# Kernel tuning notes

Hardware: AMD Instinct MI355X
Metric: run time of the kernel (lower is better)

Reference implementation:

```python
import jax, jax.numpy as jnp
import numpy as np

MAX_DUR = 8  # exclusive upper bound used when sampling durations


def setup_inputs() -> dict:
    key = jax.random.key(0)
    k1, k2 = jax.random.split(key)
    B, S, D = 16, 512, 384
    text_emb = jax.random.normal(k1, (B, S, D), dtype=jnp.float32)
    durations = jax.random.randint(k2, (B, S), 0, MAX_DUR, dtype=jnp.int32)
    return {"text_emb": text_emb, "durations": durations}


def reference(text_emb, durations):
    # text_emb: [B, S, D] float32; durations: [B, S] int32
    B, S, D = text_emb.shape
    max_len = S * MAX_DUR  # static padded length (jit-compatible stand-in for pad_sequence)
    # cumulative end offset of each token's expanded span: [B, S]
    cs = jnp.cumsum(durations, axis=1)
    t = jnp.arange(max_len, dtype=cs.dtype)  # output frame positions
    # for each output frame t, source token idx = first j with cs[j] > t
    idx = jax.vmap(lambda c: jnp.searchsorted(c, t, side="right"))(cs)  # [B, max_len]
    total = cs[:, -1:]                      # [B, 1] total expanded length per batch
    valid = t[None, :] < total              # [B, max_len] padding mask
    idx = jnp.clip(idx, 0, S - 1)
    # gather embeddings: [B, max_len, D]
    out = jnp.take_along_axis(text_emb, idx[:, :, None], axis=1)
    return jnp.where(valid[:, :, None], out, jnp.zeros((), dtype=text_emb.dtype))
```

## Files before the change

### kernel.cpp

```cpp
#include <hip/hip_runtime.h>


#define BB 16
#define SS 512
#define DD 384
#define D4 (DD / 4)
#define MAXLEN 4096
#define BATCH_F4 (MAXLEN * D4)
#define K2_ITERS 8
#define K2_CHUNK (256 * K2_ITERS)
#define CHUNKS_PER_B (BATCH_F4 / K2_CHUNK)

typedef float f32x4 __attribute__((ext_vector_type(4)));

__global__ __launch_bounds__(256)
void lr_prologue_kernel(const int* __restrict__ dur, short* __restrict__ idxmap) {
    __shared__ int cs[SS];
    const int b       = blockIdx.x >> 2;
    const int quarter = blockIdx.x & 3;
    const int tid     = threadIdx.x;

    if (tid < 64) {
        const int* drow = dur + b * SS + tid * 8;
        int loc[8];
        int run = 0;
        #pragma unroll
        for (int j = 0; j < 8; ++j) { run += drow[j]; loc[j] = run; }
        int sc = run;
        #pragma unroll
        for (int off = 1; off < 64; off <<= 1) {
            int n = __shfl_up(sc, off, 64);
            if (tid >= off) sc += n;
        }
        const int base = sc - run;
        #pragma unroll
        for (int j = 0; j < 8; ++j) cs[tid * 8 + j] = base + loc[j];
    }
    __syncthreads();

    const int total = cs[SS - 1];
    short* omap = idxmap + b * MAXLEN + quarter * 1024;
    for (int k = 0; k < 4; ++k) {
        const int t = quarter * 1024 + k * 256 + tid;
        int lo = 0, hi = SS;
        while (lo < hi) {
            int mid = (lo + hi) >> 1;
            if (cs[mid] <= t) lo = mid + 1; else hi = mid;
        }
        if (lo > SS - 1) lo = SS - 1;
        omap[k * 256 + tid] = (short)((t < total) ? lo : -1);
    }
}

__global__ __launch_bounds__(256)
void lr_gather_kernel(const f32x4* __restrict__ emb,
                      const short* __restrict__ idxmap,
                      f32x4* __restrict__ out) {
    const unsigned x   = blockIdx.x;
    const unsigned xcd = x & 7;
    const unsigned w   = x >> 3;
    const unsigned b   = xcd + 8u * (w & 1);
    const unsigned c   = w >> 1;

    const unsigned local0 = c * K2_CHUNK + threadIdx.x;
    const f32x4* embb = emb + b * (SS * D4);
    const short* imap = idxmap + b * MAXLEN;
    f32x4* outb       = out + (size_t)b * BATCH_F4;

    #pragma unroll
    for (int k = 0; k < K2_ITERS; ++k) {
        const unsigned local = local0 + k * 256;
        const unsigned bt = local / D4;
        const unsigned d4 = local - bt * D4;
        const int idx = (int)imap[bt];
        f32x4 v = {0.f, 0.f, 0.f, 0.f};
        if (idx >= 0) v = embb[(unsigned)idx * D4 + d4];
        outb[local] = v;
    }
}

extern "C" void kernel_launch(void* const* d_in, const int* in_sizes, int n_in,
                              void* d_out, int out_size, void* d_ws, size_t ws_size,
                              hipStream_t stream) {
    const float* text_emb  = (const float*)d_in[0];
    const int*   durations = (const int*)d_in[1];
    float* out = (float*)d_out;

    short* idxmap = (short*)d_ws;

    lr_prologue_kernel<<<BB * 4, 256, 0, stream>>>(durations, idxmap);

    lr_gather_kernel<<<BB * CHUNKS_PER_B, 256, 0, stream>>>(
        (const f32x4*)text_emb, idxmap, (f32x4*)out);
}
```

Before: 119.1 us.

## Fuse duration prefix-sum and index search into the gather kernel

Merges the prologue and gather kernels into a single launch. Each gather block now recomputes the prefix sum of its batch row in shared memory and binary-searches only the handful of frame indices its chunk covers. This removes a kernel launch, the inter-kernel dependency and the global index-map round trip. In exchange, every block redundantly scans 512 durations, which adds per-block latency before any stores begin.

```diff
diff --git a/kernel.cpp b/kernel.cpp
--- a/kernel.cpp
+++ b/kernel.cpp
@@ -10,15 +10,23 @@
 #define K2_ITERS 8
 #define K2_CHUNK (256 * K2_ITERS)
 #define CHUNKS_PER_B (BATCH_F4 / K2_CHUNK)
+#define MAP_ENTRIES 24
 
 typedef float f32x4 __attribute__((ext_vector_type(4)));
 
 __global__ __launch_bounds__(256)
-void lr_prologue_kernel(const int* __restrict__ dur, short* __restrict__ idxmap) {
-    __shared__ int cs[SS];
-    const int b       = blockIdx.x >> 2;
-    const int quarter = blockIdx.x & 3;
-    const int tid     = threadIdx.x;
+void lr_fused_kernel(const int* __restrict__ dur,
+                     const f32x4* __restrict__ emb,
+                     f32x4* __restrict__ out) {
+    __shared__ int   cs[SS];
+    __shared__ short smap[MAP_ENTRIES];
+
+    const unsigned x   = blockIdx.x;
+    const unsigned xcd = x & 7;
+    const unsigned w   = x >> 3;
+    const unsigned b   = xcd + 8u * (w & 1);
+    const unsigned c   = w >> 1;
+    const int tid      = threadIdx.x;
 
     if (tid < 64) {
         const int* drow = dur + b * SS + tid * 8;
@@ -38,33 +46,25 @@
     }
     __syncthreads();
 
-    const int total = cs[SS - 1];
-    short* omap = idxmap + b * MAXLEN + quarter * 1024;
-    for (int k = 0; k < 4; ++k) {
-        const int t = quarter * 1024 + k * 256 + tid;
+    const unsigned base_f4 = c * K2_CHUNK;
+    const unsigned bt0     = base_f4 / D4;
+    const unsigned lastbt  = (base_f4 + K2_CHUNK - 1) / D4;
+    const unsigned nent    = lastbt - bt0 + 1;
+    const int total        = cs[SS - 1];
+    if (tid < (int)nent) {
+        const int t = (int)bt0 + tid;
         int lo = 0, hi = SS;
         while (lo < hi) {
             int mid = (lo + hi) >> 1;
             if (cs[mid] <= t) lo = mid + 1; else hi = mid;
         }
         if (lo > SS - 1) lo = SS - 1;
-        omap[k * 256 + tid] = (short)((t < total) ? lo : -1);
+        smap[tid] = (short)((t < total) ? lo : -1);
     }
-}
+    __syncthreads();
 
-__global__ __launch_bounds__(256)
-void lr_gather_kernel(const f32x4* __restrict__ emb,
-                      const short* __restrict__ idxmap,
-                      f32x4* __restrict__ out) {
-    const unsigned x   = blockIdx.x;
-    const unsigned xcd = x & 7;
-    const unsigned w   = x >> 3;
-    const unsigned b   = xcd + 8u * (w & 1);
-    const unsigned c   = w >> 1;
-
-    const unsigned local0 = c * K2_CHUNK + threadIdx.x;
+    const unsigned local0 = base_f4 + tid;
     const f32x4* embb = emb + b * (SS * D4);
-    const short* imap = idxmap + b * MAXLEN;
     f32x4* outb       = out + (size_t)b * BATCH_F4;
 
     #pragma unroll
@@ -72,7 +72,7 @@
         const unsigned local = local0 + k * 256;
         const unsigned bt = local / D4;
         const unsigned d4 = local - bt * D4;
-        const int idx = (int)imap[bt];
+        const int idx = (int)smap[bt - bt0];
         f32x4 v = {0.f, 0.f, 0.f, 0.f};
         if (idx >= 0) v = embb[(unsigned)idx * D4 + d4];
         outb[local] = v;
@@ -85,11 +85,8 @@
     const float* text_emb  = (const float*)d_in[0];
     const int*   durations = (const int*)d_in[1];
     float* out = (float*)d_out;
+    (void)d_ws; (void)ws_size;
 
-    short* idxmap = (short*)d_ws;
-
-    lr_prologue_kernel<<<BB * 4, 256, 0, stream>>>(durations, idxmap);
-
-    lr_gather_kernel<<<BB * CHUNKS_PER_B, 256, 0, stream>>>(
-        (const f32x4*)text_emb, idxmap, (f32x4*)out);
+    lr_fused_kernel<<<BB * CHUNKS_PER_B, 256, 0, stream>>>(
+        durations, (const f32x4*)text_emb, (f32x4*)out);
 }
```

After: 116.8 us. Within noise of the previous version (-2.0%).
